# Kernel tuning notes

Hardware: AMD Instinct MI355X
Metric: run time of the kernel (lower is better)

## Reference

```python
import jax, jax.numpy as jnp
import numpy as np

ATTEN = 2  # window half-size -> 2*ATTEN+1 = 5 neighbors
B, S, IN, H, MID, OUT = 1024, 100, 100, 128, 32, 2
MAX_LEN = 100
SQRT_H = float(np.sqrt(float(H)))


def _xavier(k, i, o):
    return jax.random.normal(k, (i, o), jnp.float32) * np.sqrt(2.0 / (i + o))


def _positional_encoding():
    pos = np.arange(MAX_LEN, dtype=np.float32)[:, None]
    div = np.exp(np.arange(0, H, 2, dtype=np.float32) * (-np.log(10000.0) / H))
    pe = np.zeros((MAX_LEN, H), np.float32)
    pe[:, 0::2] = np.sin(pos * div)
    pe[:, 1::2] = np.cos(pos * div)
    return jnp.asarray(pe[None])  # (1, MAX_LEN, H)


def setup_inputs() -> dict:
    key = jax.random.key(0)
    ks = jax.random.split(key, 7)
    return {
        "x": jax.random.normal(ks[0], (B, S, IN), jnp.float32),
        "W1": _xavier(ks[1], IN, H),
        "b1": jnp.zeros((1, 1, H), jnp.float32),
        "Wq": _xavier(ks[2], H, H),
        "Wk": _xavier(ks[3], H, H),
        "Wv": _xavier(ks[4], H, H),
        "bv": jnp.zeros((1, 1, H), jnp.float32),
        "W2": _xavier(ks[5], H, MID),
        "b2": jnp.zeros((1, 1, MID), jnp.float32),
        "W3": _xavier(ks[6], MID, OUT),
        "b3": jnp.zeros((1, 1, OUT), jnp.float32),
        "pe": _positional_encoding(),
    }


def reference(x, W1, b1, Wq, Wk, Wv, bv, W2, b2, W3, b3, pe):
    seq_len = x.shape[1]
    h = jax.nn.relu(x @ W1 + b1) + pe[:, :seq_len, :]  # (B,S,H)
    # zero-pad seq dim by ATTEN on each side; torch pad+roll+stack+slice is
    # equivalent to gathering window offsets +2,+1,0,-1,-2 (in that order)
    padded = jnp.pad(h, ((0, 0), (ATTEN, ATTEN), (0, 0)))
    x_nei = jnp.stack(
        [padded[:, ATTEN - k: ATTEN - k + seq_len, :] for k in range(-ATTEN, ATTEN + 1)],
        axis=2,
    )  # (B,S,5,H); index m corresponds to neighbor x[i + ATTEN - m]
    q = h @ Wq                      # (B,S,H)
    keys = x_nei @ Wk               # (B,S,5,H)
    vals = x_nei @ Wv + bv          # (B,S,5,H)
    scores = jnp.einsum("bsh,bswh->bsw", q, keys) / SQRT_H
    w = jax.nn.softmax(scores, axis=-1)  # (B,S,5)
    context = jnp.einsum("bsw,bswh->bsh", w, vals)
    output = jax.nn.relu(context @ W2 + b2) @ W3 + b3  # (B,S,OUT)
    return output, w[:, :, None, :]  # weights shaped (B,S,1,5) like torch
```

## Files before the change

kernel.cpp:

```cpp
#include <hip/hip_runtime.h>
#include <hip/hip_bf16.h>

#define B_ 1024
#define S_ 100
#define IN_ 100
#define H_ 128
#define MID_ 32
#define OUT_ 2
#define P_ (B_ * S_)
#define RSQRT_H 0.08838834764831845f
#define LSTR 136
#define TILE 25
#define KR 32
#define HR 34

typedef __attribute__((ext_vector_type(8))) short short8;
typedef __attribute__((ext_vector_type(4))) float float4v;

__device__ __forceinline__ float bf2f(ushort u) {
    union { unsigned u; float f; } c; c.u = ((unsigned)u) << 16; return c.f;
}
__device__ __forceinline__ ushort f2bf(float x) {
    union { float f; unsigned u; } c; c.f = x;
    unsigned r = c.u + 0x7FFFu + ((c.u >> 16) & 1u);
    return (ushort)(r >> 16);
}

__global__ __launch_bounds__(256) void prep_kernel(const float* __restrict__ W1,
                                                   const float* __restrict__ Wv,
                                                   const float* __restrict__ W2,
                                                   const float* __restrict__ Wq,
                                                   const float* __restrict__ Wk,
                                                   ushort* __restrict__ W1T,
                                                   ushort* __restrict__ WvT,
                                                   ushort* __restrict__ W2T,
                                                   ushort* __restrict__ WqkT) {
    int tid = threadIdx.x;
    if (blockIdx.x < 144) {
        int g = blockIdx.x * 256 + tid;
        if (g < 16384) {
            int n = g >> 7, k = g & 127;
            W1T[g] = (k < IN_) ? f2bf(W1[k * H_ + n]) : (ushort)0;
        } else if (g < 32768) {
            int e = g - 16384; int n = e >> 7, k = e & 127;
            WvT[e] = f2bf(Wv[k * H_ + n]);
        } else {
            int e = g - 32768; int n = e >> 7, k = e & 127;
            W2T[e] = f2bf(W2[k * MID_ + n]);
        }
    } else {
        __shared__ float sq[32][132];
        __shared__ float sk[32][132];
        int bb = blockIdx.x - 144;
        int n0 = (bb >> 2) * 32, k0 = (bb & 3) * 32;
        for (int i = tid; i < 32 * 128; i += 256) {
            int r = i >> 7, c = i & 127;
            sq[r][c] = Wq[(k0 + r) * H_ + c];
            sk[r][c] = Wk[(n0 + r) * H_ + c];
        }
        __syncthreads();
        for (int i = tid; i < 1024; i += 256) {
            int kk = i & 31, nn = i >> 5;
            float a = 0.f;
            for (int j = 0; j < 128; ++j) a += sq[kk][j] * sk[nn][j];
            WqkT[(n0 + nn) * 128 + (k0 + kk)] = f2bf(a);
        }
    }
}

template <int EPI>
__device__ __forceinline__ void mm2(const ushort* __restrict__ A, int abase,
                                    const ushort* __restrict__ WT,
                                    ushort* __restrict__ C,
                                    int wave, int lane,
                                    const float* __restrict__ bias,
                                    const float* __restrict__ pe, int srow0) {
    int l15 = lane & 15, quad = lane >> 4;
    short8 bfrag[2][4];
#pragma unroll
    for (int nt = 0; nt < 2; ++nt) {
        int n = (wave * 2 + nt) * 16 + l15;
#pragma unroll
        for (int ks = 0; ks < 4; ++ks)
            bfrag[nt][ks] = *(const short8*)(WT + n * 128 + ks * 32 + quad * 8);
    }
    float biasv[2] = {0.f, 0.f};
    if (EPI != 0) {
#pragma unroll
        for (int nt = 0; nt < 2; ++nt) biasv[nt] = bias[(wave * 2 + nt) * 16 + l15];
    }
#pragma unroll
    for (int mt = 0; mt < 2; ++mt) {
        short8 afrag[4];
#pragma unroll
        for (int ks = 0; ks < 4; ++ks)
            afrag[ks] = *(const short8*)(A + (abase + mt * 16 + l15) * LSTR + ks * 32 + quad * 8);
#pragma unroll
        for (int nt = 0; nt < 2; ++nt) {
            float4v acc = {0.f, 0.f, 0.f, 0.f};
#pragma unroll
            for (int ks = 0; ks < 4; ++ks)
                acc = __builtin_amdgcn_mfma_f32_16x16x32_bf16(afrag[ks], bfrag[nt][ks], acc, 0, 0, 0);
            int n = (wave * 2 + nt) * 16 + l15;
#pragma unroll
            for (int i = 0; i < 4; ++i) {
                int row = mt * 16 + quad * 4 + i;
                float v = acc[i];
                if (EPI == 1) {
                    int srow = srow0 + row;
                    v = (srow >= 0 && srow < S_)
                            ? (fmaxf(v + biasv[nt], 0.f) + pe[srow * H_ + n]) : 0.f;
                } else if (EPI == 2) v = v + biasv[nt];
                C[row * LSTR + n] = f2bf(v);
            }
        }
    }
}

__global__ __launch_bounds__(256, 5) void fused_kernel(
    const float* __restrict__ x, const ushort* __restrict__ W1T,
    const ushort* __restrict__ WqkT, const ushort* __restrict__ WvT,
    const ushort* __restrict__ W2T,
    const float* __restrict__ b1, const float* __restrict__ bv,
    const float* __restrict__ b2, const float* __restrict__ W3,
    const float* __restrict__ b3, const float* __restrict__ pe,
    float* __restrict__ out, float* __restrict__ wout) {
    __shared__ ushort klds[KR * LSTR];
    __shared__ ushort hlds[HR * LSTR];
    __shared__ float warr[TILE * 5];

    int tid = threadIdx.x, wave = tid >> 6, lane = tid & 63;
    int b = blockIdx.x >> 2, t = blockIdx.x & 3;
    int r0 = t * TILE;
    int srow0 = r0 - 2;

    for (int i = tid; i < 29 * 18; i += 256) {
        int r = i / 18, c = 100 + 2 * (i - r * 18);
        *(uint*)(klds + r * LSTR + c) = 0u;
    }
    for (int i = tid; i < 3 * 68; i += 256) {
        int r = 29 + i / 68, c = 2 * (i % 68);
        *(uint*)(klds + r * LSTR + c) = 0u;
    }
    for (int i = tid; i < 2 * 68; i += 256) {
        int r = 32 + i / 68, c = 2 * (i % 68);
        *(uint*)(hlds + r * LSTR + c) = 0u;
    }
    {
        int g0 = srow0 < 0 ? 0 : srow0;
        int g1 = (r0 + 27 < S_) ? (r0 + 27) : S_;
        int lr0 = g0 - srow0;
        const float* xb = x + ((size_t)b * S_ + g0) * IN_;
        int pairs = (g1 - g0) * 50;
        for (int p = tid; p < pairs; p += 256) {
            int row = p / 50;
            int c2 = (p - row * 50) * 2;
            const float* src = xb + row * IN_ + c2;
            uint pk = ((uint)f2bf(src[1]) << 16) | (uint)f2bf(src[0]);
            *(uint*)(klds + (lr0 + row) * LSTR + c2) = pk;
        }
    }
    __syncthreads();
    mm2<1>(klds, 0, W1T, hlds, wave, lane, b1, pe, srow0);
    __syncthreads();
    mm2<0>(hlds, 2, WqkT, klds, wave, lane, nullptr, nullptr, 0);
    __syncthreads();
    if (tid < TILE * 8) {
        int r = tid >> 3, sub = tid & 7;
        const ushort* kqr = klds + r * LSTR + sub * 16;
        float kqf[16];
#pragma unroll
        for (int c = 0; c < 2; ++c) {
            short8 v = *(const short8*)(kqr + c * 8);
#pragma unroll
            for (int j = 0; j < 8; ++j) kqf[c * 8 + j] = bf2f((ushort)v[j]);
        }
        float sc[5];
#pragma unroll
        for (int m = 0; m < 5; ++m) {
            int gs = r0 + r + 2 - m;
            float p = 0.f;
            if (gs >= 0 && gs < S_) {
                const ushort* hr = hlds + (r + 4 - m) * LSTR + sub * 16;
#pragma unroll
                for (int c = 0; c < 2; ++c) {
                    short8 v = *(const short8*)(hr + c * 8);
#pragma unroll
                    for (int j = 0; j < 8; ++j) p += bf2f((ushort)v[j]) * kqf[c * 8 + j];
                }
            }
            sc[m] = p;
        }
#pragma unroll
        for (int m = 0; m < 5; ++m) {
            sc[m] += __shfl_xor(sc[m], 1);
            sc[m] += __shfl_xor(sc[m], 2);
            sc[m] += __shfl_xor(sc[m], 4);
            sc[m] *= RSQRT_H;
        }
        float mx = sc[0];
#pragma unroll
        for (int m = 1; m < 5; ++m) mx = fmaxf(mx, sc[m]);
        float e[5], ss = 0.f;
#pragma unroll
        for (int m = 0; m < 5; ++m) { e[m] = __expf(sc[m] - mx); ss += e[m]; }
        float inv = 1.f / ss;
        float w5[5];
#pragma unroll
        for (int m = 0; m < 5; ++m) w5[m] = e[m] * inv;
        if (sub == 0) {
#pragma unroll
            for (int m = 0; m < 5; ++m) warr[r * 5 + m] = w5[m];
        }
        float acc[16];
#pragma unroll
        for (int c = 0; c < 16; ++c) acc[c] = 0.f;
#pragma unroll
        for (int m = 0; m < 5; ++m) {
            int gs = r0 + r + 2 - m;
            if (gs < 0 || gs >= S_) continue;
            float wm = w5[m];
            const ushort* hr = hlds + (r + 4 - m) * LSTR + sub * 16;
#pragma unroll
            for (int c = 0; c < 2; ++c) {
                short8 v = *(const short8*)(hr + c * 8);
#pragma unroll
                for (int j = 0; j < 8; ++j) acc[c * 8 + j] += wm * bf2f((ushort)v[j]);
            }
        }
        ushort* op = klds + r * LSTR + sub * 16;
#pragma unroll
        for (int c = 0; c < 2; ++c) {
            short8 v;
#pragma unroll
            for (int j = 0; j < 8; ++j) v[j] = (short)f2bf(acc[c * 8 + j]);
            *(short8*)(op + c * 8) = v;
        }
    }
    __syncthreads();
    if (tid < TILE * 5)
        wout[(size_t)b * (S_ * 5) + r0 * 5 + tid] = warr[tid];
    mm2<2>(klds, 0, WvT, hlds, wave, lane, bv, nullptr, 0);
    __syncthreads();
    {
        int l15 = lane & 15, quad = lane >> 4;
        int mt = wave & 1, nt = wave >> 1;
        short8 bfrag[4];
#pragma unroll
        for (int ks = 0; ks < 4; ++ks)
            bfrag[ks] = *(const short8*)(W2T + (nt * 16 + l15) * 128 + ks * 32 + quad * 8);
        float bias2 = b2[nt * 16 + l15];
        short8 afrag[4];
#pragma unroll
        for (int ks = 0; ks < 4; ++ks)
            afrag[ks] = *(const short8*)(hlds + (mt * 16 + l15) * LSTR + ks * 32 + quad * 8);
        float4v acc = {0.f, 0.f, 0.f, 0.f};
#pragma unroll
        for (int ks = 0; ks < 4; ++ks)
            acc = __builtin_amdgcn_mfma_f32_16x16x32_bf16(afrag[ks], bfrag[ks], acc, 0, 0, 0);
#pragma unroll
        for (int i = 0; i < 4; ++i) {
            int row = mt * 16 + quad * 4 + i;
            klds[row * LSTR + nt * 16 + l15] = f2bf(fmaxf(acc[i] + bias2, 0.f));
        }
    }
    __syncthreads();
    if (tid < TILE) {
        int r = tid;
        float o0 = b3[0], o1 = b3[1];
#pragma unroll
        for (int k = 0; k < MID_; ++k) {
            float mv = bf2f(klds[r * LSTR + k]);
            o0 += mv * W3[k * 2];
            o1 += mv * W3[k * 2 + 1];
        }
        float2* op = (float2*)(out + ((size_t)b * S_ + r0 + r) * OUT_);
        *op = make_float2(o0, o1);
    }
}

extern "C" void kernel_launch(void* const* d_in, const int* in_sizes, int n_in,
                              void* d_out, int out_size, void* d_ws, size_t ws_size,
                              hipStream_t stream) {
    const float* x  = (const float*)d_in[0];
    const float* W1 = (const float*)d_in[1];
    const float* b1 = (const float*)d_in[2];
    const float* Wq = (const float*)d_in[3];
    const float* Wk = (const float*)d_in[4];
    const float* Wv = (const float*)d_in[5];
    const float* bv = (const float*)d_in[6];
    const float* W2 = (const float*)d_in[7];
    const float* b2 = (const float*)d_in[8];
    const float* W3 = (const float*)d_in[9];
    const float* b3 = (const float*)d_in[10];
    const float* pe = (const float*)d_in[11];

    float* out  = (float*)d_out;
    float* wout = out + (size_t)P_ * OUT_;

    ushort* W1T  = (ushort*)d_ws;
    ushort* WqkT = W1T + 16384;
    ushort* WvT  = WqkT + 16384;
    ushort* W2T  = WvT + 16384;

    prep_kernel<<<160, 256, 0, stream>>>(W1, Wv, W2, Wq, Wk, W1T, WvT, W2T, WqkT);
    fused_kernel<<<B_ * 4, 256, 0, stream>>>(x, W1T, WqkT, WvT, W2T,
                                             b1, bv, b2, W3, b3, pe, out, wout);
}
```

Baseline: 163.3 us.

## Compute windowed attention scores and context with MFMA via banded weight matrix

Replaces the per-thread scalar score and context loops with MFMA tiles. Scores come from a 32x32 matmul of transformed queries against h, and the diagonal band is read out for the softmax. The context is a banded weight matrix multiplied by a transposed copy of h kept in LDS. The 1/sqrt(H) scale is folded into WqkT, and the final output projection is split across two threads per row. The extra shared buffers (hT, scores, band) raise LDS use, so launch bounds drop from 5 to 4 blocks per CU, and extra syncs and some wasted MFMA work are added.

```diff
diff --git a/kernel.cpp b/kernel.cpp
--- a/kernel.cpp
+++ b/kernel.cpp
@@ -12,7 +12,10 @@
 #define LSTR 136
 #define TILE 25
 #define KR 32
-#define HR 34
+#define HR 36
+#define HTS 40
+#define SSTR 36
+#define WSTR 40
 
 typedef __attribute__((ext_vector_type(8))) short short8;
 typedef __attribute__((ext_vector_type(4))) float float4v;
@@ -63,15 +66,16 @@
             int kk = i & 31, nn = i >> 5;
             float a = 0.f;
             for (int j = 0; j < 128; ++j) a += sq[kk][j] * sk[nn][j];
-            WqkT[(n0 + nn) * 128 + (k0 + kk)] = f2bf(a);
-        }
-    }
-}
-
-template <int EPI>
+            WqkT[(n0 + nn) * 128 + (k0 + kk)] = f2bf(a * RSQRT_H);
+        }
+    }
+}
+
+template <int EPI, bool HT>
 __device__ __forceinline__ void mm2(const ushort* __restrict__ A, int abase,
                                     const ushort* __restrict__ WT,
                                     ushort* __restrict__ C,
+                                    ushort* __restrict__ hTp,
                                     int wave, int lane,
                                     const float* __restrict__ bias,
                                     const float* __restrict__ pe, int srow0) {
@@ -111,13 +115,15 @@
                     v = (srow >= 0 && srow < S_)
                             ? (fmaxf(v + biasv[nt], 0.f) + pe[srow * H_ + n]) : 0.f;
                 } else if (EPI == 2) v = v + biasv[nt];
-                C[row * LSTR + n] = f2bf(v);
+                ushort bf = f2bf(v);
+                C[row * LSTR + n] = bf;
+                if (HT) hTp[n * HTS + row] = bf;
             }
         }
     }
 }
 
-__global__ __launch_bounds__(256, 5) void fused_kernel(
+__global__ __launch_bounds__(256, 4) void fused_kernel(
     const float* __restrict__ x, const ushort* __restrict__ W1T,
     const ushort* __restrict__ WqkT, const ushort* __restrict__ WvT,
     const ushort* __restrict__ W2T,
@@ -125,11 +131,15 @@
     const float* __restrict__ b2, const float* __restrict__ W3,
     const float* __restrict__ b3, const float* __restrict__ pe,
     float* __restrict__ out, float* __restrict__ wout) {
-    __shared__ ushort klds[KR * LSTR];
-    __shared__ ushort hlds[HR * LSTR];
+    __shared__ __attribute__((aligned(16))) ushort klds[KR * LSTR];
+    __shared__ __attribute__((aligned(16))) ushort hlds[HR * LSTR];
+    __shared__ __attribute__((aligned(16))) ushort hT[H_ * HTS];
+    __shared__ __attribute__((aligned(16))) float  slds[KR * SSTR];
+    __shared__ __attribute__((aligned(16))) ushort wband[KR * WSTR];
     __shared__ float warr[TILE * 5];
 
     int tid = threadIdx.x, wave = tid >> 6, lane = tid & 63;
+    int l15 = lane & 15, quad = lane >> 4;
     int b = blockIdx.x >> 2, t = blockIdx.x & 3;
     int r0 = t * TILE;
     int srow0 = r0 - 2;
@@ -142,7 +152,7 @@
         int r = 29 + i / 68, c = 2 * (i % 68);
         *(uint*)(klds + r * LSTR + c) = 0u;
     }
-    for (int i = tid; i < 2 * 68; i += 256) {
+    for (int i = tid; i < 4 * 68; i += 256) {
         int r = 32 + i / 68, c = 2 * (i % 68);
         *(uint*)(hlds + r * LSTR + c) = 0u;
     }
@@ -161,89 +171,75 @@
         }
     }
     __syncthreads();
-    mm2<1>(klds, 0, W1T, hlds, wave, lane, b1, pe, srow0);
-    __syncthreads();
-    mm2<0>(hlds, 2, WqkT, klds, wave, lane, nullptr, nullptr, 0);
-    __syncthreads();
-    if (tid < TILE * 8) {
-        int r = tid >> 3, sub = tid & 7;
-        const ushort* kqr = klds + r * LSTR + sub * 16;
-        float kqf[16];
-#pragma unroll
-        for (int c = 0; c < 2; ++c) {
-            short8 v = *(const short8*)(kqr + c * 8);
-#pragma unroll
-            for (int j = 0; j < 8; ++j) kqf[c * 8 + j] = bf2f((ushort)v[j]);
-        }
-        float sc[5];
-#pragma unroll
-        for (int m = 0; m < 5; ++m) {
-            int gs = r0 + r + 2 - m;
-            float p = 0.f;
-            if (gs >= 0 && gs < S_) {
-                const ushort* hr = hlds + (r + 4 - m) * LSTR + sub * 16;
-#pragma unroll
-                for (int c = 0; c < 2; ++c) {
-                    short8 v = *(const short8*)(hr + c * 8);
-#pragma unroll
-                    for (int j = 0; j < 8; ++j) p += bf2f((ushort)v[j]) * kqf[c * 8 + j];
-                }
+    mm2<1, true>(klds, 0, W1T, hlds, hT, wave, lane, b1, pe, srow0);
+    __syncthreads();
+    mm2<0, false>(hlds, 2, WqkT, klds, nullptr, wave, lane, nullptr, nullptr, 0);
+    __syncthreads();
+    if (wave < 3) {
+        int qt = (wave == 2) ? 1 : 0;
+        int ht = (wave == 0) ? 0 : 1;
+        short8 afrag[4], bfrag[4];
+#pragma unroll
+        for (int ks = 0; ks < 4; ++ks) {
+            afrag[ks] = *(const short8*)(klds + (qt * 16 + l15) * LSTR + ks * 32 + quad * 8);
+            bfrag[ks] = *(const short8*)(hlds + (ht * 16 + l15) * LSTR + ks * 32 + quad * 8);
+        }
+        float4v acc = {0.f, 0.f, 0.f, 0.f};
+#pragma unroll
+        for (int ks = 0; ks < 4; ++ks)
+            acc = __builtin_amdgcn_mfma_f32_16x16x32_bf16(afrag[ks], bfrag[ks], acc, 0, 0, 0);
+#pragma unroll
+        for (int i = 0; i < 4; ++i)
+            slds[(qt * 16 + quad * 4 + i) * SSTR + ht * 16 + l15] = acc[i];
+    } else {
+        uint* wz = (uint*)wband;
+        for (int i = lane; i < (KR * WSTR) / 2; i += 64) wz[i] = 0u;
+    }
+    __syncthreads();
+    if (tid < TILE) {
+        int i = tid;
+        float sc5[5];
+#pragma unroll
+        for (int d = 0; d < 5; ++d) sc5[d] = slds[i * SSTR + i + d];
+        float mx = sc5[0];
+#pragma unroll
+        for (int d = 1; d < 5; ++d) mx = fmaxf(mx, sc5[d]);
+        float e5[5], ss = 0.f;
+#pragma unroll
+        for (int d = 0; d < 5; ++d) { e5[d] = __expf(sc5[d] - mx); ss += e5[d]; }
+        float inv = 1.f / ss;
+#pragma unroll
+        for (int d = 0; d < 5; ++d) {
+            float w = e5[d] * inv;
+            wband[i * WSTR + i + d] = f2bf(w);
+            warr[i * 5 + (4 - d)] = w;
+        }
+    }
+    __syncthreads();
+    {
+        short8 afr[2];
+        afr[0] = *(const short8*)(wband + l15 * WSTR + quad * 8);
+        afr[1] = *(const short8*)(wband + (16 + l15) * WSTR + quad * 8);
+#pragma unroll
+        for (int ntt = 0; ntt < 2; ++ntt) {
+            int n = (wave * 2 + ntt) * 16 + l15;
+            short8 bfr = *(const short8*)(hT + n * HTS + quad * 8);
+#pragma unroll
+            for (int mt = 0; mt < 2; ++mt) {
+                float4v acc = {0.f, 0.f, 0.f, 0.f};
+                acc = __builtin_amdgcn_mfma_f32_16x16x32_bf16(afr[mt], bfr, acc, 0, 0, 0);
+#pragma unroll
+                for (int i = 0; i < 4; ++i)
+                    klds[(mt * 16 + quad * 4 + i) * LSTR + n] = f2bf(acc[i]);
             }
-            sc[m] = p;
-        }
-#pragma unroll
-        for (int m = 0; m < 5; ++m) {
-            sc[m] += __shfl_xor(sc[m], 1);
-            sc[m] += __shfl_xor(sc[m], 2);
-            sc[m] += __shfl_xor(sc[m], 4);
-            sc[m] *= RSQRT_H;
-        }
-        float mx = sc[0];
-#pragma unroll
-        for (int m = 1; m < 5; ++m) mx = fmaxf(mx, sc[m]);
-        float e[5], ss = 0.f;
-#pragma unroll
-        for (int m = 0; m < 5; ++m) { e[m] = __expf(sc[m] - mx); ss += e[m]; }
-        float inv = 1.f / ss;
-        float w5[5];
-#pragma unroll
-        for (int m = 0; m < 5; ++m) w5[m] = e[m] * inv;
-        if (sub == 0) {
-#pragma unroll
-            for (int m = 0; m < 5; ++m) warr[r * 5 + m] = w5[m];
-        }
-        float acc[16];
-#pragma unroll
-        for (int c = 0; c < 16; ++c) acc[c] = 0.f;
-#pragma unroll
-        for (int m = 0; m < 5; ++m) {
-            int gs = r0 + r + 2 - m;
-            if (gs < 0 || gs >= S_) continue;
-            float wm = w5[m];
-            const ushort* hr = hlds + (r + 4 - m) * LSTR + sub * 16;
-#pragma unroll
-            for (int c = 0; c < 2; ++c) {
-                short8 v = *(const short8*)(hr + c * 8);
-#pragma unroll
-                for (int j = 0; j < 8; ++j) acc[c * 8 + j] += wm * bf2f((ushort)v[j]);
-            }
-        }
-        ushort* op = klds + r * LSTR + sub * 16;
-#pragma unroll
-        for (int c = 0; c < 2; ++c) {
-            short8 v;
-#pragma unroll
-            for (int j = 0; j < 8; ++j) v[j] = (short)f2bf(acc[c * 8 + j]);
-            *(short8*)(op + c * 8) = v;
-        }
-    }
+        }
+    }
+    __syncthreads();
+    mm2<2, false>(klds, 0, WvT, hlds, nullptr, wave, lane, bv, nullptr, 0);
     __syncthreads();
     if (tid < TILE * 5)
         wout[(size_t)b * (S_ * 5) + r0 * 5 + tid] = warr[tid];
-    mm2<2>(klds, 0, WvT, hlds, wave, lane, bv, nullptr, 0);
-    __syncthreads();
     {
-        int l15 = lane & 15, quad = lane >> 4;
         int mt = wave & 1, nt = wave >> 1;
         short8 bfrag[4];
 #pragma unroll
@@ -265,17 +261,17 @@
         }
     }
     __syncthreads();
-    if (tid < TILE) {
-        int r = tid;
-        float o0 = b3[0], o1 = b3[1];
-#pragma unroll
-        for (int k = 0; k < MID_; ++k) {
-            float mv = bf2f(klds[r * LSTR + k]);
-            o0 += mv * W3[k * 2];
-            o1 += mv * W3[k * 2 + 1];
-        }
-        float2* op = (float2*)(out + ((size_t)b * S_ + r0 + r) * OUT_);
-        *op = make_float2(o0, o1);
+    if (tid < TILE * 2) {
+        int r = tid >> 1, c = tid & 1;
+        float o = b3[c];
+        const ushort* mr = klds + r * LSTR;
+#pragma unroll
+        for (int cs = 0; cs < 4; ++cs) {
+            short8 v = *(const short8*)(mr + cs * 8);
+#pragma unroll
+            for (int j = 0; j < 8; ++j) o += bf2f((ushort)v[j]) * W3[(cs * 8 + j) * 2 + c];
+        }
+        out[((size_t)b * S_ + r0 + r) * OUT_ + c] = o;
     }
 }
 
```

New measurement: 168.2 us. +3.0%, slower.
